# Performance work log

Hardware: AMD Instinct MI355X
Metric: run time of the kernel (lower is better)

The kernel has to match this reference:

```python
import jax, jax.numpy as jnp
import numpy as np
from jax import lax

B_SZ, C_IN, C_OUT, H_IM, W_IM = 2, 128, 128, 64, 64
N_STATE = 16
DT_RANK = 4  # ceil(128/32)


def _ln_cf(x, w, b, eps=1e-6):
    # channels_first LayerNorm over channel dim
    u = x.mean(1, keepdims=True)
    s = ((x - u) ** 2).mean(1, keepdims=True)
    return w[None, :, None, None] * (x - u) / jnp.sqrt(s + eps) + b[None, :, None, None]


def _bn_train(x, g, b, eps=1e-5):
    # BatchNorm2d in training mode (batch statistics, biased variance)
    m = x.mean((0, 2, 3), keepdims=True)
    v = ((x - m) ** 2).mean((0, 2, 3), keepdims=True)
    return g[None, :, None, None] * (x - m) / jnp.sqrt(v + eps) + b[None, :, None, None]


def _dwconv(x, w, b):
    y = lax.conv_general_dilated(x, w, (1, 1), 'SAME', feature_group_count=x.shape[1],
                                 dimension_numbers=('NCHW', 'OIHW', 'NCHW'))
    return y + b[None, :, None, None]


def _conv1x1(x, w, b):
    return jnp.einsum('oi,bihw->bohw', w, x) + b[None, :, None, None]


def _selective_scan(u, dt, A, Bm, Cm, D, delta_bias):
    # u, dt: [B,Ch,L]; A: [Ch,N]; Bm, Cm: [B,N,L]; D: [Ch]
    dt = jax.nn.softplus(dt + delta_bias[None, :, None])
    xs = (dt.transpose(2, 0, 1), u.transpose(2, 0, 1), Bm.transpose(2, 0, 1), Cm.transpose(2, 0, 1))
    h0 = jnp.zeros(u.shape[:2] + (A.shape[1],), u.dtype)

    def step(h, inp):
        dt_t, u_t, b_t, c_t = inp
        dA = jnp.exp(dt_t[..., None] * A)                        # [B,Ch,N]
        h = h * dA + (dt_t * u_t)[..., None] * b_t[:, None, :]   # [B,Ch,N]
        return h, jnp.einsum('bcn,bn->bc', h, c_t)

    _, ys = lax.scan(step, h0, xs)
    return ys.transpose(1, 2, 0) + u * D[None, :, None]


def _ssm_apply(u, Wx, bx, Wdt, bdt, Alog, D, r):
    # u: [B,Ch,L]. Replicates torch row-major .reshape of [(B L),D] -> [B,D,L].
    Bb, Ch, L = u.shape
    N = Alog.shape[1]
    x_flat = u.transpose(0, 2, 1).reshape(Bb * L, Ch)   # 'b c l -> (b l) c'
    x_dbl = x_flat @ Wx.T + bx
    dt = (x_dbl[:, :r] @ Wdt.T + bdt).reshape(Bb, Wdt.shape[0], L)
    Bm = x_dbl[:, r:r + N].reshape(Bb, N, L)
    Cm = x_dbl[:, r + N:].reshape(Bb, N, L)
    return _selective_scan(u, dt, -jnp.exp(Alog), Bm, Cm, D, bdt)


def _forward(x, ln_in_w, ln_in_b, inproj_w, inproj_b, ln_mamba_w, ln_mamba_b, convm_w, convm_b,
             convr_w, convr_b, ln_cat_w, ln_cat_b, xproj_f_w, xproj_f_b, dtproj_f_w, dtproj_f_b,
             Alog_f, D_f, xproj_b_w, xproj_b_b, dtproj_b_w, dtproj_b_b, Alog_b, D_b,
             xproj_u_w, xproj_u_b, dtproj_u_w, dtproj_u_b, Alog_u, D_u, gate1_w, gate1_b,
             bn_g, bn_b, gate2_w, gate2_b, outproj_w, outproj_b, outln_w, outln_b):
    Bb, C, H, W = x.shape
    L = H * W
    half = C // 2
    x = _ln_cf(x, ln_in_w, ln_in_b)
    xp = _conv1x1(x, inproj_w, inproj_b)
    x_mamba, x_res = xp[:, :C], xp[:, C:]
    x_mamba = _ln_cf(x_mamba, ln_mamba_w, ln_mamba_b)
    x_mamba = jax.nn.silu(_dwconv(x_mamba, convm_w, convm_b))
    x_res = jax.nn.silu(_dwconv(x_res, convr_w, convr_b))
    # forward scan on first half of channels
    xf = x_mamba[:, :half].reshape(Bb, half, L)
    yf = _ssm_apply(xf, xproj_f_w, xproj_f_b, dtproj_f_w, dtproj_f_b, Alog_f, D_f, DT_RANK).reshape(Bb, half, H, W)
    # backward scan on second half (flip H,W, scan, flip back)
    xb = x_mamba[:, half:][:, :, ::-1, ::-1]
    yb = _ssm_apply(xb.reshape(Bb, half, L), xproj_b_w, xproj_b_b, dtproj_b_w, dtproj_b_b,
                    Alog_b, D_b, DT_RANK).reshape(Bb, half, H, W)[:, :, ::-1, ::-1]
    concat = _ln_cf(jnp.concatenate([yf, yb], axis=1), ln_cat_w, ln_cat_b)
    # uncertainty-ordered scan on full x_mamba
    sig = jax.nn.sigmoid(x_mamba.mean(1, keepdims=True))
    unc = (-(sig * jnp.log(sig + 1e-6))).reshape(Bb, L)
    idx = jnp.argsort(-unc, axis=1)       # descending uncertainty
    inv = jnp.argsort(idx, axis=1)        # inverse permutation
    xs = jnp.take_along_axis(x_mamba.reshape(Bb, C, L), idx[:, None, :], axis=2)
    yu = _ssm_apply(xs, xproj_u_w, xproj_u_b, dtproj_u_w, dtproj_u_b, Alog_u, D_u, 2 * DT_RANK)
    yu = jnp.take_along_axis(yu, inv[:, None, :], axis=2).reshape(Bb, C, H, W)
    # gated fusion
    g = jax.nn.relu(_bn_train(_conv1x1(jnp.concatenate([concat, yu], 1), gate1_w, gate1_b), bn_g, bn_b))
    g = jax.nn.sigmoid(_conv1x1(g, gate2_w, gate2_b))
    fused = g * yu + (1.0 - g) * concat
    out = _conv1x1(jnp.concatenate([fused, x_res], 1), outproj_w, outproj_b)
    return _ln_cf(out, outln_w, outln_b)


def setup_inputs() -> dict:
    key = jax.random.key(0)
    ks = jax.random.split(key, 16)
    C, half, R, N = C_IN, C_IN // 2, DT_RANK, N_STATE
    rn = lambda k, shp, s=0.02: jax.random.normal(k, shp, jnp.float32) * s

    def inv_dt(k, n):
        dt = jnp.exp(jax.random.uniform(k, (n,)) * (np.log(0.1) - np.log(0.001)) + np.log(0.001))
        dt = jnp.maximum(dt, 1e-4)
        return dt + jnp.log(-jnp.expm1(-dt))

    std = R ** -0.5
    Alog_h = jnp.log(jnp.broadcast_to(jnp.arange(1, N + 1, dtype=jnp.float32), (half, N)))
    Alog_fl = jnp.log(jnp.broadcast_to(jnp.arange(1, N + 1, dtype=jnp.float32), (C, N)))
    return {
        'x': jax.random.normal(ks[0], (B_SZ, C, H_IM, W_IM), jnp.float32),
        'ln_in_w': jnp.ones(C), 'ln_in_b': jnp.zeros(C),
        'inproj_w': rn(ks[1], (2 * C, C)), 'inproj_b': jnp.zeros(2 * C),
        'ln_mamba_w': jnp.ones(C), 'ln_mamba_b': jnp.zeros(C),
        'convm_w': rn(ks[2], (C, 1, 3, 3), 0.1), 'convm_b': jnp.zeros(C),
        'convr_w': rn(ks[3], (C, 1, 3, 3), 0.1), 'convr_b': jnp.zeros(C),
        'ln_cat_w': jnp.ones(C), 'ln_cat_b': jnp.zeros(C),
        'xproj_f_w': rn(ks[4], (R + 2 * N, half)), 'xproj_f_b': jnp.zeros(R + 2 * N),
        'dtproj_f_w': jax.random.uniform(ks[5], (half, R), minval=-std, maxval=std),
        'dtproj_f_b': inv_dt(ks[6], half),
        'Alog_f': Alog_h, 'D_f': jnp.ones(half),
        'xproj_b_w': rn(ks[7], (R + 2 * N, half)), 'xproj_b_b': jnp.zeros(R + 2 * N),
        'dtproj_b_w': jax.random.uniform(ks[8], (half, R), minval=-std, maxval=std),
        'dtproj_b_b': inv_dt(ks[9], half),
        'Alog_b': Alog_h, 'D_b': jnp.ones(half),
        'xproj_u_w': rn(ks[10], (2 * R + 2 * N, C)), 'xproj_u_b': jnp.zeros(2 * R + 2 * N),
        'dtproj_u_w': jax.random.uniform(ks[11], (C, 2 * R), minval=-std, maxval=std),
        'dtproj_u_b': inv_dt(ks[12], C),
        'Alog_u': Alog_fl, 'D_u': jnp.ones(C),
        'gate1_w': rn(ks[13], (C, 2 * C)), 'gate1_b': jnp.zeros(C),
        'bn_g': jnp.ones(C), 'bn_b': jnp.zeros(C),
        'gate2_w': rn(ks[14], (C, C)), 'gate2_b': jnp.zeros(C),
        'outproj_w': rn(ks[15], (C_OUT, 2 * C)), 'outproj_b': jnp.zeros(C_OUT),
        'outln_w': jnp.ones(C_OUT), 'outln_b': jnp.zeros(C_OUT),
    }


def reference(x, ln_in_w, ln_in_b, inproj_w, inproj_b, ln_mamba_w, ln_mamba_b, convm_w, convm_b,
              convr_w, convr_b, ln_cat_w, ln_cat_b, xproj_f_w, xproj_f_b, dtproj_f_w, dtproj_f_b,
              Alog_f, D_f, xproj_b_w, xproj_b_b, dtproj_b_w, dtproj_b_b, Alog_b, D_b,
              xproj_u_w, xproj_u_b, dtproj_u_w, dtproj_u_b, Alog_u, D_u, gate1_w, gate1_b,
              bn_g, bn_b, gate2_w, gate2_b, outproj_w, outproj_b, outln_w, outln_b):
    return _forward(x, ln_in_w, ln_in_b, inproj_w, inproj_b, ln_mamba_w, ln_mamba_b, convm_w, convm_b,
                    convr_w, convr_b, ln_cat_w, ln_cat_b, xproj_f_w, xproj_f_b, dtproj_f_w, dtproj_f_b,
                    Alog_f, D_f, xproj_b_w, xproj_b_b, dtproj_b_w, dtproj_b_b, Alog_b, D_b,
                    xproj_u_w, xproj_u_b, dtproj_u_w, dtproj_u_b, Alog_u, D_u, gate1_w, gate1_b,
                    bn_g, bn_b, gate2_w, gate2_b, outproj_w, outproj_b, outln_w, outln_b)
```

## Files before the change

### kernel.cpp

```cpp
#include <hip/hip_runtime.h>
#include <cstdint>
#include <cstddef>

#define TPB 256

namespace {

constexpr int B_SZ = 2;
constexpr int C    = 128;
constexpr int HALF = 64;
constexpr int L    = 4096;
constexpr int N    = 16;
constexpr int HH   = 64;
constexpr int WW   = 64;

__device__ __forceinline__ float softplusf(float x) {
  return fmaxf(x, 0.f) + __logf(1.f + __expf(-fabsf(x)));
}
__device__ __forceinline__ float sigm(float x) { return 1.f / (1.f + __expf(-x)); }

__device__ __forceinline__ unsigned long long unc_key(float u, int i) {
  unsigned m = __float_as_uint(u);
  m = (m & 0x80000000u) ? ~m : (m | 0x80000000u);
  return ((unsigned long long)(~m) << 32) | (unsigned)i;
}

__global__ void k_conv_ln(const float* __restrict__ X, int bsX,
                          const float* __restrict__ lnw, const float* __restrict__ lnb,
                          const float* __restrict__ W, const float* __restrict__ bias,
                          float* __restrict__ Y, int I, int O,
                          float* __restrict__ st1s, float* __restrict__ st1q) {
  constexpr int O_PB = 8;
  __shared__ float Wl[O_PB * 128];
  __shared__ float aw[128], ab[128];
  const int o0 = blockIdx.y * O_PB;
  const int b  = blockIdx.z;
  for (int t = threadIdx.x; t < O_PB * I; t += TPB) {
    int i = t / O_PB, k = t % O_PB;
    Wl[t] = W[(size_t)(o0 + k) * I + i];
  }
  for (int t = threadIdx.x; t < I; t += TPB) { aw[t] = lnw[t]; ab[t] = lnb[t]; }
  __syncthreads();
  const int l0 = blockIdx.x * (2 * TPB) + threadIdx.x;
  const int l1 = l0 + TPB;
  const float* X0 = X + (size_t)b * bsX + l0;
  const float* X1 = X + (size_t)b * bsX + l1;
  float s0 = 0.f, q0 = 0.f, s1 = 0.f, q1 = 0.f;
#pragma unroll 8
  for (int i = 0; i < I; ++i) {
    float v0 = X0[(size_t)i * L], v1 = X1[(size_t)i * L];
    s0 += v0; q0 += v0 * v0; s1 += v1; q1 += v1 * v1;
  }
  const float m0 = s0 / I, m1 = s1 / I;
  const float r0 = rsqrtf(q0 / I - m0 * m0 + 1e-6f);
  const float r1 = rsqrtf(q1 / I - m1 * m1 + 1e-6f);
  float acc0[O_PB], acc1[O_PB];
#pragma unroll
  for (int k = 0; k < O_PB; ++k) { acc0[k] = bias[o0 + k]; acc1[k] = acc0[k]; }
#pragma unroll 4
  for (int i = 0; i < I; ++i) {
    float xv0 = (X0[(size_t)i * L] - m0) * r0 * aw[i] + ab[i];
    float xv1 = (X1[(size_t)i * L] - m1) * r1 * aw[i] + ab[i];
#pragma unroll
    for (int k = 0; k < O_PB; ++k) {
      acc0[k] += Wl[i * O_PB + k] * xv0;
      acc1[k] += Wl[i * O_PB + k] * xv1;
    }
  }
#pragma unroll
  for (int k = 0; k < O_PB; ++k) {
    Y[((size_t)b * O + o0 + k) * L + l0] = acc0[k];
    Y[((size_t)b * O + o0 + k) * L + l1] = acc1[k];
  }
  if (o0 < 128) {
    float ss0 = 0.f, qq0 = 0.f, ss1 = 0.f, qq1 = 0.f;
#pragma unroll
    for (int k = 0; k < O_PB; ++k) {
      ss0 += acc0[k]; qq0 += acc0[k] * acc0[k];
      ss1 += acc1[k]; qq1 += acc1[k] * acc1[k];
    }
    atomicAdd(&st1s[b * L + l0], ss0);
    atomicAdd(&st1q[b * L + l0], qq0);
    atomicAdd(&st1s[b * L + l1], ss1);
    atomicAdd(&st1q[b * L + l1], qq1);
  }
}

__global__ void k_dwconv_t(const float* __restrict__ xp,
                           const float* __restrict__ st1s, const float* __restrict__ st1q,
                           const float* __restrict__ lnw, const float* __restrict__ lnb,
                           const float* __restrict__ Wm, const float* __restrict__ bm,
                           const float* __restrict__ Wr, const float* __restrict__ br,
                           float* __restrict__ xm, float* __restrict__ xr) {
  const int c = blockIdx.y;
  const int z = blockIdx.z;
  const int b = z & 1, mode = z >> 1;
  const int h0 = blockIdx.x * 4;
  __shared__ float T[6][66];
  const float* Xc = xp + ((size_t)b * 2 * C + (mode ? C + c : c)) * L;
  const float lw = mode ? 0.f : lnw[c];
  const float lb2 = mode ? 0.f : lnb[c];
  for (int t = threadIdx.x; t < 6 * 66; t += TPB) {
    int r = t / 66, cc = t % 66 - 1;
    int hh = h0 - 1 + r;
    float v = 0.f;
    if (hh >= 0 && hh < HH && cc >= 0 && cc < WW) {
      int li = hh * WW + cc;
      v = Xc[li];
      if (mode == 0) {
        float sv = st1s[b * L + li], qv = st1q[b * L + li];
        float m = sv * (1.f / 128.f);
        float rr = rsqrtf(qv * (1.f / 128.f) - m * m + 1e-6f);
        v = (v - m) * rr * lw + lb2;
      }
    }
    T[r][t % 66] = v;
  }
  __syncthreads();
  const int hl = threadIdx.x >> 6, w = threadIdx.x & 63;
  const float* W9 = (mode ? Wr : Wm) + c * 9;
  float acc = mode ? br[c] : bm[c];
#pragma unroll
  for (int kh = 0; kh < 3; ++kh)
#pragma unroll
    for (int kw = 0; kw < 3; ++kw)
      acc += T[hl + kh][w + kw] * W9[kh * 3 + kw];
  const int l = (h0 + hl) * WW + w;
  float* Yp = mode ? xr : xm;
  Yp[((size_t)b * C + c) * L + l] = acc * sigm(acc);
}

__global__ void k_unc(const float* __restrict__ xm, float* __restrict__ unc) {
  const int lp = threadIdx.x & 31;
  const int g  = threadIdx.x >> 5;
  const int p  = blockIdx.x * 32 + lp;
  const int b = p / L, l = p % L;
  const float* Xp = xm + (size_t)b * C * L + l;
  float s = 0.f;
#pragma unroll 8
  for (int i = 0; i < 16; ++i) s += Xp[(size_t)(g * 16 + i) * L];
  __shared__ float r1[8][32];
  r1[g][lp] = s;
  __syncthreads();
  if (g == 0) {
    float st = 0.f;
#pragma unroll
    for (int j = 0; j < 8; ++j) st += r1[j][lp];
    float sg = sigm(st / C);
    unc[p] = -(sg * __logf(sg + 1e-6f));
  }
}

__global__ void k_rank(const float* __restrict__ unc, int* __restrict__ rankbuf) {
  constexpr int JC = 512;
  __shared__ unsigned long long K[JC];
  const int b  = blockIdx.z;
  const int j0 = blockIdx.y * JC;
  const int i  = blockIdx.x * TPB + threadIdx.x;
  for (int t = threadIdx.x; t < JC; t += TPB)
    K[t] = unc_key(unc[b * L + j0 + t], j0 + t);
  __syncthreads();
  const unsigned long long my = unc_key(unc[b * L + i], i);
  int cnt = 0;
#pragma unroll 8
  for (int j = 0; j < JC; ++j) cnt += (K[j] < my) ? 1 : 0;
  atomicAdd(&rankbuf[b * L + i], cnt);
}

__global__ void k_scatgath(const float* __restrict__ xm, const int* __restrict__ rankbuf,
                           float* __restrict__ xs, int* __restrict__ inv,
                           int* __restrict__ idx) {
  int t = blockIdx.x * TPB + threadIdx.x;
  int l = t % L, c = (t / L) % C, b = t / (C * L);
  int r = rankbuf[b * L + l];
  xs[((size_t)b * C + c) * L + r] = xm[t];
  if (c == 0) { inv[b * L + l] = r; idx[b * L + r] = l; }
}

__global__ void k_convx_all(const float* __restrict__ xm, const float* __restrict__ xs,
                            const float* __restrict__ Wf, const float* __restrict__ bf,
                            const float* __restrict__ Wb, const float* __restrict__ bb,
                            const float* __restrict__ Wu, const float* __restrict__ bu,
                            float* __restrict__ XDF, float* __restrict__ XDU) {
  constexpr int O_PB = 8;
  const int z = blockIdx.z;
  const bool isU = z >= 4;
  const int I = isU ? 128 : 64;
  const int O = isU ? 40 : 36;
  const int o0 = blockIdx.y * O_PB;
  if (o0 >= O) return;
  int b, dir;
  const float *W, *bi;
  if (!isU) { dir = z >> 1; b = z & 1; W = dir ? Wb : Wf; bi = dir ? bb : bf; }
  else      { dir = 0; b = z - 4; W = Wu; bi = bu; }
  __shared__ float Wl[O_PB * 128];
  for (int t = threadIdx.x; t < O_PB * I; t += TPB) {
    int i = t / O_PB, k = t % O_PB;
    Wl[t] = (o0 + k < O) ? W[(size_t)(o0 + k) * I + i] : 0.f;
  }
  __syncthreads();
  const int l = blockIdx.x * TPB + threadIdx.x;
  const int ls = isU ? l : (dir ? (L - 1 - l) : l);
  const float* Xb = isU ? (xs + (size_t)b * C * L)
                        : (xm + ((size_t)b * C + dir * HALF) * L);
  float acc[O_PB];
#pragma unroll
  for (int k = 0; k < O_PB; ++k) acc[k] = (o0 + k < O) ? bi[o0 + k] : 0.f;
#pragma unroll 4
  for (int i = 0; i < I; ++i) {
    float xv = Xb[(size_t)i * L + ls];
#pragma unroll
    for (int k = 0; k < O_PB; ++k) acc[k] += Wl[i * O_PB + k] * xv;
  }
  float* yp = isU ? (XDU + ((size_t)b * L + l) * 40 + o0)
                  : (XDF + ((size_t)z * L + l) * 36 + o0);
#pragma unroll
  for (int k = 0; k < O_PB; ++k)
    if (o0 + k < O) yp[k] = acc[k];
}

__global__ void k_bc_all(const float* __restrict__ xdblF, const float* __restrict__ xdblU,
                         float* __restrict__ BmTF, float* __restrict__ CmTF,
                         float* __restrict__ BmTU, float* __restrict__ CmTU) {
  const int z = blockIdx.z;
  const bool isU = z >= 4;
  const int RT = isU ? 8 : 4, OT = isU ? 40 : 36;
  const float* src = isU ? (xdblU + (size_t)(z - 4) * L * 40)
                         : (xdblF + (size_t)z * L * 36);
  float* BT = isU ? (BmTU + (size_t)(z - 4) * L * N) : (BmTF + (size_t)z * L * N);
  float* CT = isU ? (CmTU + (size_t)(z - 4) * L * N) : (CmTF + (size_t)z * L * N);
  const int n = blockIdx.y;
  const int l2 = blockIdx.x * TPB + threadIdx.x;
  int f2 = n * L + l2;
  int lb = f2 >> 4, cb = f2 & 15;
  const float* xr2 = src + (size_t)lb * OT + RT + cb;
  size_t ob = (size_t)l2 * N + n;
  BT[ob] = xr2[0];
  CT[ob] = xr2[N];
}

__global__ __launch_bounds__(1024) void
k_scan_all(const float* __restrict__ xdblF, const float* __restrict__ xdblU,
           const float* __restrict__ dtf_w, const float* __restrict__ dtf_b,
           const float* __restrict__ dtb_w, const float* __restrict__ dtb_b,
           const float* __restrict__ dtu_w, const float* __restrict__ dtu_b,
           const float* __restrict__ xm, const float* __restrict__ xs,
           const int* __restrict__ idx,
           const float* __restrict__ BmTF, const float* __restrict__ CmTF,
           const float* __restrict__ BmTU, const float* __restrict__ CmTU,
           const float* __restrict__ Alog_f, const float* __restrict__ Alog_b,
           const float* __restrict__ Alog_u,
           const float* __restrict__ D_f, const float* __restrict__ D_b,
           const float* __restrict__ D_u,
           float* __restrict__ yf, float* __restrict__ yb, float* __restrict__ yu) {
  const int blk = blockIdx.x;
  const int tid = threadIdx.x;
  const bool isU = blk >= 256;
  int CsT, RT, c, b, dir;
  const float *Wdt, *bdt, *Alog, *Dv, *xdbl, *BT, *CT, *Ub;
  const int* idxb = nullptr;
  float* Y;
  int OT;
  if (!isU) {
    CsT = 64; RT = 4; OT = 36;
    int zb = blk >> 6; c = blk & 63; dir = zb >> 1; b = zb & 1;
    Wdt = dir ? dtb_w : dtf_w; bdt = dir ? dtb_b : dtf_b;
    Alog = dir ? Alog_b : Alog_f; Dv = dir ? D_b : D_f;
    xdbl = xdblF + (size_t)zb * L * 36;
    BT = BmTF + (size_t)zb * L * N; CT = CmTF + (size_t)zb * L * N;
    Ub = xm + ((size_t)b * C + dir * HALF + c) * L;
    Y = (dir ? yb : yf) + ((size_t)b * HALF + c) * L;
  } else {
    CsT = 128; RT = 8; OT = 40;
    int blk2 = blk - 256; b = blk2 >> 7; c = blk2 & 127; dir = 0;
    Wdt = dtu_w; bdt = dtu_b; Alog = Alog_u; Dv = D_u;
    xdbl = xdblU + (size_t)b * L * 40;
    BT = BmTU + (size_t)b * L * N; CT = CmTU + (size_t)b * L * N;
    Ub = xs + ((size_t)b * C + c) * L;
    idxb = idx + b * L;
    Y = yu + ((size_t)b * C + c) * L;
  }
  __shared__ float sW[1024];
  __shared__ float sb2[128];
  __shared__ float4 dtL4[64 * 17];
  __shared__ float4 uL4[64 * 17];
  __shared__ float sA[N][65], sH[N][65];
  for (int t = tid; t < CsT * RT; t += 1024) {
    int csrc = t / RT, r = t % RT;
    sW[r * CsT + csrc] = Wdt[t];
  }
  for (int t = tid; t < CsT; t += 1024) sb2[t] = bdt[t];
  __syncthreads();
  {
    const int chunk_d = tid >> 4;
    const int sq4 = tid & 15;
    const int sq = sq4 * 4;
    const int lsrc = isU ? (c * 32 + (chunk_d >> 1)) : (c * 64 + chunk_d);
    const float* xrp = xdbl + (size_t)lsrc * OT;
    float xr[8];
    for (int r = 0; r < RT; ++r) xr[r] = xrp[r];
    const float bcc = sb2[c];
    float dv[4], uv[4];
#pragma unroll
    for (int j = 0; j < 4; ++j) {
      int s = sq + j;
      int csrc = isU ? (((chunk_d & 1) << 6) + s) : s;
      float acc = sb2[csrc] + bcc;
      for (int r = 0; r < RT; ++r) acc += sW[r * CsT + csrc] * xr[r];
      int l = (chunk_d << 6) + s;
      dv[j] = softplusf(acc);
      uv[j] = Ub[isU ? l : (dir ? (L - 1 - l) : l)];
    }
    dtL4[chunk_d * 17 + sq4] = make_float4(dv[0], dv[1], dv[2], dv[3]);
    uL4[chunk_d * 17 + sq4]  = make_float4(uv[0], uv[1], uv[2], uv[3]);
  }
  __syncthreads();
  const int n = tid & 15;
  const int chunk = tid >> 4;
  const float a = -__expf(Alog[c * N + n]);
  const float* bp = BT + ((size_t)(chunk << 6)) * N + n;
  const float* cp = CT + ((size_t)(chunk << 6)) * N + n;
  float ap = 1.f, h = 0.f;
#pragma unroll 4
  for (int m = 0; m < 16; ++m) {
    float4 d4 = dtL4[chunk * 17 + m];
    float4 u4 = uL4[chunk * 17 + m];
    float dv[4] = {d4.x, d4.y, d4.z, d4.w};
    float uv[4] = {u4.x, u4.y, u4.z, u4.w};
#pragma unroll
    for (int jj = 0; jj < 4; ++jj) {
      int s = (m << 2) + jj;
      float bn = bp[(size_t)s * N];
      float dA = __expf(dv[jj] * a);
      ap *= dA;
      h = h * dA + dv[jj] * uv[jj] * bn;
    }
  }
  sA[n][chunk] = ap; sH[n][chunk] = h;
  __syncthreads();
  {
    const int w = tid >> 6;
    const int k = tid & 63;
    float A = sA[w][k];
    float Bv = sH[w][k];
#pragma unroll
    for (int j = 1; j < 64; j <<= 1) {
      float pa = __shfl_up(A, j);
      float pb = __shfl_up(Bv, j);
      if (k >= j) { Bv = pb * A + Bv; A = pa * A; }
    }
    float hprev = __shfl_up(Bv, 1);
    sH[w][k] = (k == 0) ? 0.f : hprev;
  }
  __syncthreads();
  h = sH[n][chunk];
  const float Dc = Dv[c];
  const float* uLrow = (const float*)&uL4[chunk * 17];
  const bool h1 = (n & 1) != 0, h2 = (n & 2) != 0, h3 = (n & 4) != 0, h4 = (n & 8) != 0;
  float ybuf[4];
#pragma unroll
  for (int q = 0; q < 4; ++q) {
    float v[16];
#pragma unroll
    for (int m = 0; m < 4; ++m) {
      float4 d4 = dtL4[chunk * 17 + (q << 2) + m];
      float4 u4 = uL4[chunk * 17 + (q << 2) + m];
      float dv[4] = {d4.x, d4.y, d4.z, d4.w};
      float uv[4] = {u4.x, u4.y, u4.z, u4.w};
#pragma unroll
      for (int jj = 0; jj < 4; ++jj) {
        int s = (q << 4) + (m << 2) + jj;
        float bn = bp[(size_t)s * N];
        float cn = cp[(size_t)s * N];
        float dA = __expf(dv[jj] * a);
        h = h * dA + dv[jj] * uv[jj] * bn;
        v[(m << 2) + jj] = h * cn;
      }
    }
    float u8[8];
#pragma unroll
    for (int k2 = 0; k2 < 8; ++k2) {
      float snd = h1 ? v[2 * k2] : v[2 * k2 + 1];
      float t = __shfl_xor(snd, 1);
      u8[k2] = (h1 ? v[2 * k2 + 1] : v[2 * k2]) + t;
    }
    float u4a[4];
#pragma unroll
    for (int k2 = 0; k2 < 4; ++k2) {
      float snd = h2 ? u8[2 * k2] : u8[2 * k2 + 1];
      float t = __shfl_xor(snd, 2);
      u4a[k2] = (h2 ? u8[2 * k2 + 1] : u8[2 * k2]) + t;
    }
    float u2a[2];
#pragma unroll
    for (int k2 = 0; k2 < 2; ++k2) {
      float snd = h3 ? u4a[2 * k2] : u4a[2 * k2 + 1];
      float t = __shfl_xor(snd, 4);
      u2a[k2] = (h3 ? u4a[2 * k2 + 1] : u4a[2 * k2]) + t;
    }
    float snd = h4 ? u2a[0] : u2a[1];
    float t = __shfl_xor(snd, 8);
    float ysum = (h4 ? u2a[1] : u2a[0]) + t;
    float myu = uLrow[(q << 4) + n];
    ybuf[q] = ysum + myu * Dc;
  }
  if (!isU) {
    float* Yp = Y + (chunk << 6);
#pragma unroll
    for (int q = 0; q < 4; ++q) Yp[16 * q + n] = ybuf[q];
  } else {
    const int s0 = chunk << 6;
#pragma unroll
    for (int q = 0; q < 4; ++q) Y[idxb[s0 + 16 * q + n]] = ybuf[q];
  }
}

template <int O_PB>
__global__ void k_gate1(const float* __restrict__ yf, const float* __restrict__ yb,
                        const float* __restrict__ lncw, const float* __restrict__ lncb,
                        const float* __restrict__ yu,
                        const float* __restrict__ W, const float* __restrict__ bias,
                        float* __restrict__ g1,
                        float* __restrict__ st2m, float* __restrict__ st2r,
                        float* __restrict__ bnsum) {
  __shared__ float Wl[O_PB * 256];
  __shared__ float cw[128], cb2[128];
  __shared__ float part[2][O_PB][4];
  const int o0 = blockIdx.y * O_PB;
  const int b  = blockIdx.z;
  for (int t = threadIdx.x; t < O_PB * 256; t += TPB) {
    int i = t / O_PB, k = t % O_PB;
    Wl[t] = W[(size_t)(o0 + k) * 256 + i];
  }
  for (int t = threadIdx.x; t < 128; t += TPB) { cw[t] = lncw[t]; cb2[t] = lncb[t]; }
  __syncthreads();
  const int l = blockIdx.x * TPB + threadIdx.x;
  const float* f0 = yf + (size_t)b * HALF * L + l;
  const float* b0 = yb + (size_t)b * HALF * L + (L - 1 - l);
  const float* u0 = yu + (size_t)b * C * L + l;
  float s = 0.f, s2 = 0.f;
#pragma unroll 8
  for (int i = 0; i < 64; ++i) { float v = f0[(size_t)i * L]; s += v; s2 += v * v; }
#pragma unroll 8
  for (int i = 0; i < 64; ++i) { float v = b0[(size_t)i * L]; s += v; s2 += v * v; }
  const float m = s / C;
  const float r = rsqrtf(s2 / C - m * m + 1e-6f);
  if (blockIdx.y == 0) { st2m[b * L + l] = m; st2r[b * L + l] = r; }
  float acc[O_PB];
#pragma unroll
  for (int k = 0; k < O_PB; ++k) acc[k] = bias[o0 + k];
#pragma unroll 4
  for (int i = 0; i < 64; ++i) {
    float cv = (f0[(size_t)i * L] - m) * r * cw[i] + cb2[i];
#pragma unroll
    for (int k = 0; k < O_PB; ++k) acc[k] += Wl[i * O_PB + k] * cv;
  }
#pragma unroll 4
  for (int i = 0; i < 64; ++i) {
    float cv = (b0[(size_t)i * L] - m) * r * cw[64 + i] + cb2[64 + i];
#pragma unroll
    for (int k = 0; k < O_PB; ++k) acc[k] += Wl[(64 + i) * O_PB + k] * cv;
  }
#pragma unroll 4
  for (int i = 0; i < 128; ++i) {
    float xv = u0[(size_t)i * L];
#pragma unroll
    for (int k = 0; k < O_PB; ++k) acc[k] += Wl[(128 + i) * O_PB + k] * xv;
  }
#pragma unroll
  for (int k = 0; k < O_PB; ++k)
    g1[((size_t)b * C + o0 + k) * L + l] = acc[k];
  const int wv = threadIdx.x >> 6, lnn = threadIdx.x & 63;
#pragma unroll
  for (int k = 0; k < O_PB; ++k) {
    float v = acc[k];
    v += __shfl_xor(v, 1);  v += __shfl_xor(v, 2);  v += __shfl_xor(v, 4);
    v += __shfl_xor(v, 8);  v += __shfl_xor(v, 16); v += __shfl_xor(v, 32);
    if (lnn == 0) part[0][k][wv] = v;
    float q = acc[k] * acc[k];
    q += __shfl_xor(q, 1);  q += __shfl_xor(q, 2);  q += __shfl_xor(q, 4);
    q += __shfl_xor(q, 8);  q += __shfl_xor(q, 16); q += __shfl_xor(q, 32);
    if (lnn == 0) part[1][k][wv] = q;
  }
  __syncthreads();
  if (threadIdx.x < 2 * O_PB) {
    int which = threadIdx.x >= O_PB, k = threadIdx.x % O_PB;
    float v = part[which][k][0] + part[which][k][1] + part[which][k][2] + part[which][k][3];
    atomicAdd(&bnsum[which * 128 + o0 + k], v);
  }
}

template <int O_PB>
__global__ void k_gate2_fuse(const float* __restrict__ g1,
                             const float* __restrict__ bnsum,
                             const float* __restrict__ bn_g, const float* __restrict__ bn_b,
                             const float* __restrict__ W, const float* __restrict__ bias,
                             const float* __restrict__ yu,
                             const float* __restrict__ yf, const float* __restrict__ yb,
                             const float* __restrict__ mean2, const float* __restrict__ rinv2,
                             const float* __restrict__ lncw, const float* __restrict__ lncb,
                             float* __restrict__ fused) {
  __shared__ float Wl[O_PB * 128];
  __shared__ float sc[128], sh[128];
  __shared__ float cwo[O_PB], cbo[O_PB];
  const int o0 = blockIdx.y * O_PB;
  const int b  = blockIdx.z;
  for (int t = threadIdx.x; t < O_PB * 128; t += TPB) {
    int i = t / O_PB, k = t % O_PB;
    Wl[t] = W[(size_t)(o0 + k) * 128 + i];
  }
  for (int t = threadIdx.x; t < 128; t += TPB) {
    float sv = bnsum[t], qv = bnsum[128 + t];
    float mean = sv / (B_SZ * L);
    float var  = qv / (B_SZ * L) - mean * mean;
    float scv = bn_g[t] * rsqrtf(var + 1e-5f);
    sc[t] = scv;
    sh[t] = bn_b[t] - mean * scv;
  }
  if (threadIdx.x < O_PB) {
    cwo[threadIdx.x] = lncw[o0 + threadIdx.x];
    cbo[threadIdx.x] = lncb[o0 + threadIdx.x];
  }
  __syncthreads();
  const int l = blockIdx.x * TPB + threadIdx.x;
  const float m = mean2[b * L + l], r = rinv2[b * L + l];
  const float* Xb = g1 + (size_t)b * C * L + l;
  float acc[O_PB];
#pragma unroll
  for (int k = 0; k < O_PB; ++k) acc[k] = bias[o0 + k];
#pragma unroll 4
  for (int i = 0; i < 128; ++i) {
    float v = fmaxf(Xb[(size_t)i * L] * sc[i] + sh[i], 0.f);
#pragma unroll
    for (int k = 0; k < O_PB; ++k) acc[k] += Wl[i * O_PB + k] * v;
  }
#pragma unroll
  for (int k = 0; k < O_PB; ++k) {
    int o = o0 + k;
    float g = sigm(acc[k]);
    float yuv = yu[((size_t)b * C + o) * L + l];
    float yv = (o < 64) ? yf[((size_t)b * HALF + o) * L + l]
                        : yb[((size_t)b * HALF + (o - 64)) * L + (L - 1 - l)];
    float cv = (yv - m) * r * cwo[k] + cbo[k];
    fused[((size_t)b * C + o) * L + l] = g * yuv + (1.f - g) * cv;
  }
}

template <int O_PB>
__global__ void k_conv1x1_cat2(const float* __restrict__ X1, const float* __restrict__ X2,
                               const float* __restrict__ W, const float* __restrict__ bias,
                               float* __restrict__ Y, int O,
                               float* __restrict__ st3s, float* __restrict__ st3q) {
  __shared__ float Wl[O_PB * 256];
  const int o0 = blockIdx.y * O_PB;
  const int b  = blockIdx.z;
  for (int t = threadIdx.x; t < O_PB * 256; t += TPB) {
    int i = t / O_PB, k = t % O_PB;
    Wl[t] = W[(size_t)(o0 + k) * 256 + i];
  }
  __syncthreads();
  const int l = blockIdx.x * TPB + threadIdx.x;
  const float* Xb1 = X1 + (size_t)b * C * L + l;
  const float* Xb2 = X2 + (size_t)b * C * L + l;
  float acc[O_PB];
#pragma unroll
  for (int k = 0; k < O_PB; ++k) acc[k] = bias[o0 + k];
#pragma unroll 4
  for (int i = 0; i < 128; ++i) {
    float xv = Xb1[(size_t)i * L];
#pragma unroll
    for (int k = 0; k < O_PB; ++k) acc[k] += Wl[i * O_PB + k] * xv;
  }
#pragma unroll 4
  for (int i = 0; i < 128; ++i) {
    float xv = Xb2[(size_t)i * L];
#pragma unroll
    for (int k = 0; k < O_PB; ++k) acc[k] += Wl[(128 + i) * O_PB + k] * xv;
  }
#pragma unroll
  for (int k = 0; k < O_PB; ++k)
    Y[((size_t)b * O + o0 + k) * L + l] = acc[k];
  float ss = 0.f, qq = 0.f;
#pragma unroll
  for (int k = 0; k < O_PB; ++k) { ss += acc[k]; qq += acc[k] * acc[k]; }
  atomicAdd(&st3s[b * L + l], ss);
  atomicAdd(&st3q[b * L + l], qq);
}

__global__ void k_ln_fin(const float* __restrict__ X,
                         const float* __restrict__ st3s, const float* __restrict__ st3q,
                         const float* __restrict__ w, const float* __restrict__ bchan,
                         float* __restrict__ Y) {
  int t = blockIdx.x * TPB + threadIdx.x;
  int l = t % L, c = (t / L) % C, b = t / (C * L);
  float m = st3s[b * L + l] * (1.f / 128.f);
  float rinv = rsqrtf(st3q[b * L + l] * (1.f / 128.f) - m * m + 1e-6f);
  Y[t] = w[c] * (X[t] - m) * rinv + bchan[c];
}

}

extern "C" void kernel_launch(void* const* d_in, const int* in_sizes, int n_in,
                              void* d_out, int out_size, void* d_ws, size_t ws_size,
                              hipStream_t stream) {
  const float* x         = (const float*)d_in[0];
  const float* ln_in_w   = (const float*)d_in[1];
  const float* ln_in_b   = (const float*)d_in[2];
  const float* inproj_w  = (const float*)d_in[3];
  const float* inproj_b  = (const float*)d_in[4];
  const float* ln_m_w    = (const float*)d_in[5];
  const float* ln_m_b    = (const float*)d_in[6];
  const float* convm_w   = (const float*)d_in[7];
  const float* convm_b   = (const float*)d_in[8];
  const float* convr_w   = (const float*)d_in[9];
  const float* convr_b   = (const float*)d_in[10];
  const float* ln_cat_w  = (const float*)d_in[11];
  const float* ln_cat_b  = (const float*)d_in[12];
  const float* xpf_w     = (const float*)d_in[13];
  const float* xpf_b     = (const float*)d_in[14];
  const float* dtf_w     = (const float*)d_in[15];
  const float* dtf_b     = (const float*)d_in[16];
  const float* Alog_f    = (const float*)d_in[17];
  const float* D_f       = (const float*)d_in[18];
  const float* xpb_w     = (const float*)d_in[19];
  const float* xpb_b     = (const float*)d_in[20];
  const float* dtb_w     = (const float*)d_in[21];
  const float* dtb_b     = (const float*)d_in[22];
  const float* Alog_b    = (const float*)d_in[23];
  const float* D_b       = (const float*)d_in[24];
  const float* xpu_w     = (const float*)d_in[25];
  const float* xpu_b     = (const float*)d_in[26];
  const float* dtu_w     = (const float*)d_in[27];
  const float* dtu_b     = (const float*)d_in[28];
  const float* Alog_u    = (const float*)d_in[29];
  const float* D_u       = (const float*)d_in[30];
  const float* gate1_w   = (const float*)d_in[31];
  const float* gate1_b   = (const float*)d_in[32];
  const float* bn_g      = (const float*)d_in[33];
  const float* bn_b      = (const float*)d_in[34];
  const float* gate2_w   = (const float*)d_in[35];
  const float* gate2_b   = (const float*)d_in[36];
  const float* outproj_w = (const float*)d_in[37];
  const float* outproj_b = (const float*)d_in[38];
  const float* outln_w   = (const float*)d_in[39];
  const float* outln_b   = (const float*)d_in[40];

  float* ws = (float*)d_ws;
  size_t off = 0;
  auto alloc = [&](size_t n) { float* p = ws + off; off += n; return p; };

  const size_t BL = (size_t)B_SZ * L;
  float* st1s  = alloc(BL);
  float* st1q  = alloc(BL);
  int*   rank  = (int*)alloc(BL);
  float* st3s  = alloc(BL);
  float* st3q  = alloc(BL);
  float* bnsum = alloc(256);
  const size_t zeroBytes = (5 * BL + 256) * sizeof(float);

  float* xp    = alloc((size_t)B_SZ * 2 * C * L);
  float* xm    = alloc((size_t)B_SZ * C * L);
  float* xr    = alloc((size_t)B_SZ * C * L);
  float* unc   = alloc(BL);
  int*   inv   = (int*)alloc(BL);
  int*   idx   = (int*)alloc(BL);
  float* xs    = alloc((size_t)B_SZ * C * L);
  float* xdblF = alloc((size_t)4 * L * 36);
  float* BmTF  = alloc((size_t)4 * L * N);
  float* CmTF  = alloc((size_t)4 * L * N);
  float* xdblU = alloc((size_t)2 * L * 40);
  float* BmTU  = alloc((size_t)2 * L * N);
  float* CmTU  = alloc((size_t)2 * L * N);
  float* yf    = alloc((size_t)B_SZ * HALF * L);
  float* yb    = alloc((size_t)B_SZ * HALF * L);
  float* yu    = alloc((size_t)B_SZ * C * L);
  float* st2m  = alloc(BL);
  float* st2r  = alloc(BL);
  float* g1    = alloc((size_t)B_SZ * C * L);
  float* fused = alloc((size_t)B_SZ * C * L);
  float* outp  = alloc((size_t)B_SZ * C * L);
  (void)ws_size; (void)in_sizes; (void)n_in; (void)out_size;

  const int elemB = B_SZ * C * L / TPB;

  hipMemsetAsync(st1s, 0, zeroBytes, stream);
  k_conv_ln<<<dim3(L / (2 * TPB), 32, B_SZ), TPB, 0, stream>>>(
      x, C * L, ln_in_w, ln_in_b, inproj_w, inproj_b, xp, 128, 256, st1s, st1q);
  k_dwconv_t<<<dim3(HH / 4, C, 2 * B_SZ), TPB, 0, stream>>>(
      xp, st1s, st1q, ln_m_w, ln_m_b, convm_w, convm_b, convr_w, convr_b, xm, xr);
  k_unc<<<B_SZ * L / 32, TPB, 0, stream>>>(xm, unc);
  k_rank<<<dim3(L / TPB, 8, B_SZ), TPB, 0, stream>>>(unc, rank);
  k_scatgath<<<elemB, TPB, 0, stream>>>(xm, rank, xs, inv, idx);
  k_convx_all<<<dim3(L / TPB, 5, 6), TPB, 0, stream>>>(
      xm, xs, xpf_w, xpf_b, xpb_w, xpb_b, xpu_w, xpu_b, xdblF, xdblU);
  k_bc_all<<<dim3(L / TPB, N, 6), TPB, 0, stream>>>(
      xdblF, xdblU, BmTF, CmTF, BmTU, CmTU);
  k_scan_all<<<512, 1024, 0, stream>>>(
      xdblF, xdblU, dtf_w, dtf_b, dtb_w, dtb_b, dtu_w, dtu_b,
      xm, xs, idx, BmTF, CmTF, BmTU, CmTU,
      Alog_f, Alog_b, Alog_u, D_f, D_b, D_u, yf, yb, yu);
  k_gate1<8><<<dim3(L / TPB, 16, B_SZ), TPB, 0, stream>>>(
      yf, yb, ln_cat_w, ln_cat_b, yu, gate1_w, gate1_b, g1, st2m, st2r, bnsum);
  k_gate2_fuse<8><<<dim3(L / TPB, 16, B_SZ), TPB, 0, stream>>>(
      g1, bnsum, bn_g, bn_b, gate2_w, gate2_b, yu, yf, yb, st2m, st2r,
      ln_cat_w, ln_cat_b, fused);
  k_conv1x1_cat2<8><<<dim3(L / TPB, 16, B_SZ), TPB, 0, stream>>>(
      fused, xr, outproj_w, outproj_b, outp, 128, st3s, st3q);
  k_ln_fin<<<elemB, TPB, 0, stream>>>(outp, st3s, st3q, outln_w, outln_b,
                                      (float*)d_out);
}
```

Before: 330.1 us.

## Merge sort pipeline and epilogue stages into cooperative kernels with grid sync

Measured after the change: 743.3 us. +125.2%, slower.

```diff
diff --git a/kernel.cpp b/kernel.cpp
--- a/kernel.cpp
+++ b/kernel.cpp
@@ -1,8 +1,11 @@
 #include <hip/hip_runtime.h>
+#include <hip/hip_cooperative_groups.h>
 #include <cstdint>
 #include <cstddef>
 
 #define TPB 256
+
+namespace cg = cooperative_groups;
 
 namespace {
 
@@ -130,51 +133,58 @@
   Yp[((size_t)b * C + c) * L + l] = acc * sigm(acc);
 }
 
-__global__ void k_unc(const float* __restrict__ xm, float* __restrict__ unc) {
-  const int lp = threadIdx.x & 31;
-  const int g  = threadIdx.x >> 5;
-  const int p  = blockIdx.x * 32 + lp;
-  const int b = p / L, l = p % L;
-  const float* Xp = xm + (size_t)b * C * L + l;
-  float s = 0.f;
+__global__ void k_sortpipe(const float* __restrict__ xm, float* __restrict__ unc,
+                           int* __restrict__ rankbuf, float* __restrict__ xs,
+                           int* __restrict__ inv, int* __restrict__ idx) {
+  cg::grid_group grid = cg::this_grid();
+  const int tid = threadIdx.x;
+  const int blk = blockIdx.x;
+  {
+    const int lp = tid & 31;
+    const int g  = tid >> 5;
+    const int p  = blk * 32 + lp;
+    const int b = p / L, l = p % L;
+    const float* Xp = xm + (size_t)b * C * L + l;
+    float s = 0.f;
 #pragma unroll 8
-  for (int i = 0; i < 16; ++i) s += Xp[(size_t)(g * 16 + i) * L];
-  __shared__ float r1[8][32];
-  r1[g][lp] = s;
-  __syncthreads();
-  if (g == 0) {
-    float st = 0.f;
-#pragma unroll
-    for (int j = 0; j < 8; ++j) st += r1[j][lp];
-    float sg = sigm(st / C);
-    unc[p] = -(sg * __logf(sg + 1e-6f));
-  }
-}
-
-__global__ void k_rank(const float* __restrict__ unc, int* __restrict__ rankbuf) {
-  constexpr int JC = 512;
-  __shared__ unsigned long long K[JC];
-  const int b  = blockIdx.z;
-  const int j0 = blockIdx.y * JC;
-  const int i  = blockIdx.x * TPB + threadIdx.x;
-  for (int t = threadIdx.x; t < JC; t += TPB)
-    K[t] = unc_key(unc[b * L + j0 + t], j0 + t);
-  __syncthreads();
-  const unsigned long long my = unc_key(unc[b * L + i], i);
-  int cnt = 0;
+    for (int i = 0; i < 16; ++i) s += Xp[(size_t)(g * 16 + i) * L];
+    __shared__ float r1[8][32];
+    r1[g][lp] = s;
+    __syncthreads();
+    if (g == 0) {
+      float st = 0.f;
+#pragma unroll
+      for (int j = 0; j < 8; ++j) st += r1[j][lp];
+      float sg = sigm(st / C);
+      unc[p] = -(sg * __logf(sg + 1e-6f));
+    }
+  }
+  __threadfence();
+  grid.sync();
+  {
+    const int b  = blk >> 7;
+    const int xg = blk & 15;
+    const int jy = (blk >> 4) & 7;
+    const int j0 = jy * 512;
+    const int i  = xg * TPB + tid;
+    __shared__ unsigned long long K[512];
+    for (int t = tid; t < 512; t += TPB)
+      K[t] = unc_key(unc[b * L + j0 + t], j0 + t);
+    __syncthreads();
+    const unsigned long long my = unc_key(unc[b * L + i], i);
+    int cnt = 0;
 #pragma unroll 8
-  for (int j = 0; j < JC; ++j) cnt += (K[j] < my) ? 1 : 0;
-  atomicAdd(&rankbuf[b * L + i], cnt);
-}
-
-__global__ void k_scatgath(const float* __restrict__ xm, const int* __restrict__ rankbuf,
-                           float* __restrict__ xs, int* __restrict__ inv,
-                           int* __restrict__ idx) {
-  int t = blockIdx.x * TPB + threadIdx.x;
-  int l = t % L, c = (t / L) % C, b = t / (C * L);
-  int r = rankbuf[b * L + l];
-  xs[((size_t)b * C + c) * L + r] = xm[t];
-  if (c == 0) { inv[b * L + l] = r; idx[b * L + r] = l; }
+    for (int j = 0; j < 512; ++j) cnt += (K[j] < my) ? 1 : 0;
+    atomicAdd(&rankbuf[b * L + i], cnt);
+  }
+  __threadfence();
+  grid.sync();
+  for (int t = blk * TPB + tid; t < B_SZ * C * L; t += 256 * TPB) {
+    int l = t % L, c = (t / L) % C, b = t / (C * L);
+    int r = rankbuf[b * L + l];
+    xs[((size_t)b * C + c) * L + r] = xm[t];
+    if (c == 0) { inv[b * L + l] = r; idx[b * L + r] = l; }
+  }
 }
 
 __global__ void k_convx_all(const float* __restrict__ xm, const float* __restrict__ xs,
@@ -415,187 +425,185 @@
   }
 }
 
-template <int O_PB>
-__global__ void k_gate1(const float* __restrict__ yf, const float* __restrict__ yb,
-                        const float* __restrict__ lncw, const float* __restrict__ lncb,
-                        const float* __restrict__ yu,
-                        const float* __restrict__ W, const float* __restrict__ bias,
-                        float* __restrict__ g1,
-                        float* __restrict__ st2m, float* __restrict__ st2r,
-                        float* __restrict__ bnsum) {
-  __shared__ float Wl[O_PB * 256];
-  __shared__ float cw[128], cb2[128];
-  __shared__ float part[2][O_PB][4];
-  const int o0 = blockIdx.y * O_PB;
-  const int b  = blockIdx.z;
-  for (int t = threadIdx.x; t < O_PB * 256; t += TPB) {
-    int i = t / O_PB, k = t % O_PB;
-    Wl[t] = W[(size_t)(o0 + k) * 256 + i];
-  }
-  for (int t = threadIdx.x; t < 128; t += TPB) { cw[t] = lncw[t]; cb2[t] = lncb[t]; }
-  __syncthreads();
-  const int l = blockIdx.x * TPB + threadIdx.x;
-  const float* f0 = yf + (size_t)b * HALF * L + l;
-  const float* b0 = yb + (size_t)b * HALF * L + (L - 1 - l);
-  const float* u0 = yu + (size_t)b * C * L + l;
-  float s = 0.f, s2 = 0.f;
+__global__ void k_epilogue(const float* __restrict__ yf, const float* __restrict__ yb,
+                           const float* __restrict__ lncw, const float* __restrict__ lncb,
+                           const float* __restrict__ yu,
+                           const float* __restrict__ g1w, const float* __restrict__ g1b,
+                           float* __restrict__ g1,
+                           float* __restrict__ st2m, float* __restrict__ st2r,
+                           float* __restrict__ bnsum,
+                           const float* __restrict__ bn_g, const float* __restrict__ bn_b,
+                           const float* __restrict__ g2w, const float* __restrict__ g2b,
+                           float* __restrict__ fused,
+                           const float* __restrict__ xr,
+                           const float* __restrict__ opw, const float* __restrict__ opb,
+                           float* __restrict__ outp,
+                           float* __restrict__ st3s, float* __restrict__ st3q,
+                           const float* __restrict__ olnw, const float* __restrict__ olnb,
+                           float* __restrict__ OUT) {
+  cg::grid_group grid = cg::this_grid();
+  constexpr int O_PB = 8;
+  const int xb = blockIdx.x & 15;
+  const int yb2 = (blockIdx.x >> 4) & 15;
+  const int b  = blockIdx.x >> 8;
+  const int o0 = yb2 * O_PB;
+  const int l  = xb * TPB + threadIdx.x;
+
+  {
+    __shared__ float Wl[O_PB * 256];
+    __shared__ float cw[128], cb2[128];
+    __shared__ float part[2][O_PB][4];
+    for (int t = threadIdx.x; t < O_PB * 256; t += TPB) {
+      int i = t / O_PB, k = t % O_PB;
+      Wl[t] = g1w[(size_t)(o0 + k) * 256 + i];
+    }
+    for (int t = threadIdx.x; t < 128; t += TPB) { cw[t] = lncw[t]; cb2[t] = lncb[t]; }
+    __syncthreads();
+    const float* f0 = yf + (size_t)b * HALF * L + l;
+    const float* b0 = yb + (size_t)b * HALF * L + (L - 1 - l);
+    const float* u0 = yu + (size_t)b * C * L + l;
+    float s = 0.f, s2 = 0.f;
 #pragma unroll 8
-  for (int i = 0; i < 64; ++i) { float v = f0[(size_t)i * L]; s += v; s2 += v * v; }
+    for (int i = 0; i < 64; ++i) { float v = f0[(size_t)i * L]; s += v; s2 += v * v; }
 #pragma unroll 8
-  for (int i = 0; i < 64; ++i) { float v = b0[(size_t)i * L]; s += v; s2 += v * v; }
-  const float m = s / C;
-  const float r = rsqrtf(s2 / C - m * m + 1e-6f);
-  if (blockIdx.y == 0) { st2m[b * L + l] = m; st2r[b * L + l] = r; }
-  float acc[O_PB];
-#pragma unroll
-  for (int k = 0; k < O_PB; ++k) acc[k] = bias[o0 + k];
-#pragma unroll 4
-  for (int i = 0; i < 64; ++i) {
-    float cv = (f0[(size_t)i * L] - m) * r * cw[i] + cb2[i];
-#pragma unroll
-    for (int k = 0; k < O_PB; ++k) acc[k] += Wl[i * O_PB + k] * cv;
-  }
-#pragma unroll 4
-  for (int i = 0; i < 64; ++i) {
-    float cv = (b0[(size_t)i * L] - m) * r * cw[64 + i] + cb2[64 + i];
-#pragma unroll
-    for (int k = 0; k < O_PB; ++k) acc[k] += Wl[(64 + i) * O_PB + k] * cv;
-  }
-#pragma unroll 4
-  for (int i = 0; i < 128; ++i) {
-    float xv = u0[(size_t)i * L];
-#pragma unroll
-    for (int k = 0; k < O_PB; ++k) acc[k] += Wl[(128 + i) * O_PB + k] * xv;
-  }
-#pragma unroll
-  for (int k = 0; k < O_PB; ++k)
-    g1[((size_t)b * C + o0 + k) * L + l] = acc[k];
-  const int wv = threadIdx.x >> 6, lnn = threadIdx.x & 63;
-#pragma unroll
-  for (int k = 0; k < O_PB; ++k) {
-    float v = acc[k];
-    v += __shfl_xor(v, 1);  v += __shfl_xor(v, 2);  v += __shfl_xor(v, 4);
-    v += __shfl_xor(v, 8);  v += __shfl_xor(v, 16); v += __shfl_xor(v, 32);
-    if (lnn == 0) part[0][k][wv] = v;
-    float q = acc[k] * acc[k];
-    q += __shfl_xor(q, 1);  q += __shfl_xor(q, 2);  q += __shfl_xor(q, 4);
-    q += __shfl_xor(q, 8);  q += __shfl_xor(q, 16); q += __shfl_xor(q, 32);
-    if (lnn == 0) part[1][k][wv] = q;
-  }
-  __syncthreads();
-  if (threadIdx.x < 2 * O_PB) {
-    int which = threadIdx.x >= O_PB, k = threadIdx.x % O_PB;
-    float v = part[which][k][0] + part[which][k][1] + part[which][k][2] + part[which][k][3];
-    atomicAdd(&bnsum[which * 128 + o0 + k], v);
-  }
-}
-
-template <int O_PB>
-__global__ void k_gate2_fuse(const float* __restrict__ g1,
-                             const float* __restrict__ bnsum,
-                             const float* __restrict__ bn_g, const float* __restrict__ bn_b,
-                             const float* __restrict__ W, const float* __restrict__ bias,
-                             const float* __restrict__ yu,
-                             const float* __restrict__ yf, const float* __restrict__ yb,
-                             const float* __restrict__ mean2, const float* __restrict__ rinv2,
-                             const float* __restrict__ lncw, const float* __restrict__ lncb,
-                             float* __restrict__ fused) {
-  __shared__ float Wl[O_PB * 128];
-  __shared__ float sc[128], sh[128];
-  __shared__ float cwo[O_PB], cbo[O_PB];
-  const int o0 = blockIdx.y * O_PB;
-  const int b  = blockIdx.z;
-  for (int t = threadIdx.x; t < O_PB * 128; t += TPB) {
-    int i = t / O_PB, k = t % O_PB;
-    Wl[t] = W[(size_t)(o0 + k) * 128 + i];
-  }
-  for (int t = threadIdx.x; t < 128; t += TPB) {
-    float sv = bnsum[t], qv = bnsum[128 + t];
-    float mean = sv / (B_SZ * L);
-    float var  = qv / (B_SZ * L) - mean * mean;
-    float scv = bn_g[t] * rsqrtf(var + 1e-5f);
-    sc[t] = scv;
-    sh[t] = bn_b[t] - mean * scv;
-  }
-  if (threadIdx.x < O_PB) {
-    cwo[threadIdx.x] = lncw[o0 + threadIdx.x];
-    cbo[threadIdx.x] = lncb[o0 + threadIdx.x];
-  }
-  __syncthreads();
-  const int l = blockIdx.x * TPB + threadIdx.x;
-  const float m = mean2[b * L + l], r = rinv2[b * L + l];
-  const float* Xb = g1 + (size_t)b * C * L + l;
-  float acc[O_PB];
-#pragma unroll
-  for (int k = 0; k < O_PB; ++k) acc[k] = bias[o0 + k];
-#pragma unroll 4
-  for (int i = 0; i < 128; ++i) {
-    float v = fmaxf(Xb[(size_t)i * L] * sc[i] + sh[i], 0.f);
-#pragma unroll
-    for (int k = 0; k < O_PB; ++k) acc[k] += Wl[i * O_PB + k] * v;
-  }
-#pragma unroll
-  for (int k = 0; k < O_PB; ++k) {
-    int o = o0 + k;
-    float g = sigm(acc[k]);
-    float yuv = yu[((size_t)b * C + o) * L + l];
-    float yv = (o < 64) ? yf[((size_t)b * HALF + o) * L + l]
-                        : yb[((size_t)b * HALF + (o - 64)) * L + (L - 1 - l)];
-    float cv = (yv - m) * r * cwo[k] + cbo[k];
-    fused[((size_t)b * C + o) * L + l] = g * yuv + (1.f - g) * cv;
-  }
-}
-
-template <int O_PB>
-__global__ void k_conv1x1_cat2(const float* __restrict__ X1, const float* __restrict__ X2,
-                               const float* __restrict__ W, const float* __restrict__ bias,
-                               float* __restrict__ Y, int O,
-                               float* __restrict__ st3s, float* __restrict__ st3q) {
-  __shared__ float Wl[O_PB * 256];
-  const int o0 = blockIdx.y * O_PB;
-  const int b  = blockIdx.z;
-  for (int t = threadIdx.x; t < O_PB * 256; t += TPB) {
-    int i = t / O_PB, k = t % O_PB;
-    Wl[t] = W[(size_t)(o0 + k) * 256 + i];
-  }
-  __syncthreads();
-  const int l = blockIdx.x * TPB + threadIdx.x;
-  const float* Xb1 = X1 + (size_t)b * C * L + l;
-  const float* Xb2 = X2 + (size_t)b * C * L + l;
-  float acc[O_PB];
-#pragma unroll
-  for (int k = 0; k < O_PB; ++k) acc[k] = bias[o0 + k];
-#pragma unroll 4
-  for (int i = 0; i < 128; ++i) {
-    float xv = Xb1[(size_t)i * L];
-#pragma unroll
-    for (int k = 0; k < O_PB; ++k) acc[k] += Wl[i * O_PB + k] * xv;
-  }
-#pragma unroll 4
-  for (int i = 0; i < 128; ++i) {
-    float xv = Xb2[(size_t)i * L];
-#pragma unroll
-    for (int k = 0; k < O_PB; ++k) acc[k] += Wl[(128 + i) * O_PB + k] * xv;
-  }
-#pragma unroll
-  for (int k = 0; k < O_PB; ++k)
-    Y[((size_t)b * O + o0 + k) * L + l] = acc[k];
-  float ss = 0.f, qq = 0.f;
-#pragma unroll
-  for (int k = 0; k < O_PB; ++k) { ss += acc[k]; qq += acc[k] * acc[k]; }
-  atomicAdd(&st3s[b * L + l], ss);
-  atomicAdd(&st3q[b * L + l], qq);
-}
-
-__global__ void k_ln_fin(const float* __restrict__ X,
-                         const float* __restrict__ st3s, const float* __restrict__ st3q,
-                         const float* __restrict__ w, const float* __restrict__ bchan,
-                         float* __restrict__ Y) {
-  int t = blockIdx.x * TPB + threadIdx.x;
-  int l = t % L, c = (t / L) % C, b = t / (C * L);
-  float m = st3s[b * L + l] * (1.f / 128.f);
-  float rinv = rsqrtf(st3q[b * L + l] * (1.f / 128.f) - m * m + 1e-6f);
-  Y[t] = w[c] * (X[t] - m) * rinv + bchan[c];
+    for (int i = 0; i < 64; ++i) { float v = b0[(size_t)i * L]; s += v; s2 += v * v; }
+    const float m = s / C;
+    const float r = rsqrtf(s2 / C - m * m + 1e-6f);
+    if (yb2 == 0) { st2m[b * L + l] = m; st2r[b * L + l] = r; }
+    float acc[O_PB];
+#pragma unroll
+    for (int k = 0; k < O_PB; ++k) acc[k] = g1b[o0 + k];
+#pragma unroll 4
+    for (int i = 0; i < 64; ++i) {
+      float cv = (f0[(size_t)i * L] - m) * r * cw[i] + cb2[i];
+#pragma unroll
+      for (int k = 0; k < O_PB; ++k) acc[k] += Wl[i * O_PB + k] * cv;
+    }
+#pragma unroll 4
+    for (int i = 0; i < 64; ++i) {
+      float cv = (b0[(size_t)i * L] - m) * r * cw[64 + i] + cb2[64 + i];
+#pragma unroll
+      for (int k = 0; k < O_PB; ++k) acc[k] += Wl[(64 + i) * O_PB + k] * cv;
+    }
+#pragma unroll 4
+    for (int i = 0; i < 128; ++i) {
+      float xv = u0[(size_t)i * L];
+#pragma unroll
+      for (int k = 0; k < O_PB; ++k) acc[k] += Wl[(128 + i) * O_PB + k] * xv;
+    }
+#pragma unroll
+    for (int k = 0; k < O_PB; ++k)
+      g1[((size_t)b * C + o0 + k) * L + l] = acc[k];
+    const int wv = threadIdx.x >> 6, lnn = threadIdx.x & 63;
+#pragma unroll
+    for (int k = 0; k < O_PB; ++k) {
+      float v = acc[k];
+      v += __shfl_xor(v, 1);  v += __shfl_xor(v, 2);  v += __shfl_xor(v, 4);
+      v += __shfl_xor(v, 8);  v += __shfl_xor(v, 16); v += __shfl_xor(v, 32);
+      if (lnn == 0) part[0][k][wv] = v;
+      float q = acc[k] * acc[k];
+      q += __shfl_xor(q, 1);  q += __shfl_xor(q, 2);  q += __shfl_xor(q, 4);
+      q += __shfl_xor(q, 8);  q += __shfl_xor(q, 16); q += __shfl_xor(q, 32);
+      if (lnn == 0) part[1][k][wv] = q;
+    }
+    __syncthreads();
+    if (threadIdx.x < 2 * O_PB) {
+      int which = threadIdx.x >= O_PB, k = threadIdx.x % O_PB;
+      float v = part[which][k][0] + part[which][k][1] + part[which][k][2] + part[which][k][3];
+      atomicAdd(&bnsum[which * 128 + o0 + k], v);
+    }
+  }
+  __threadfence();
+  grid.sync();
+
+  {
+    __shared__ float Wl2[O_PB * 128];
+    __shared__ float sc[128], sh[128];
+    __shared__ float cwo[O_PB], cbo[O_PB];
+    for (int t = threadIdx.x; t < O_PB * 128; t += TPB) {
+      int i = t / O_PB, k = t % O_PB;
+      Wl2[t] = g2w[(size_t)(o0 + k) * 128 + i];
+    }
+    for (int t = threadIdx.x; t < 128; t += TPB) {
+      float sv = bnsum[t], qv = bnsum[128 + t];
+      float mean = sv / (B_SZ * L);
+      float var  = qv / (B_SZ * L) - mean * mean;
+      float scv = bn_g[t] * rsqrtf(var + 1e-5f);
+      sc[t] = scv;
+      sh[t] = bn_b[t] - mean * scv;
+    }
+    if (threadIdx.x < O_PB) {
+      cwo[threadIdx.x] = lncw[o0 + threadIdx.x];
+      cbo[threadIdx.x] = lncb[o0 + threadIdx.x];
+    }
+    __syncthreads();
+    const float m = st2m[b * L + l], r = st2r[b * L + l];
+    const float* Xb = g1 + (size_t)b * C * L + l;
+    float acc[O_PB];
+#pragma unroll
+    for (int k = 0; k < O_PB; ++k) acc[k] = g2b[o0 + k];
+#pragma unroll 4
+    for (int i = 0; i < 128; ++i) {
+      float v = fmaxf(Xb[(size_t)i * L] * sc[i] + sh[i], 0.f);
+#pragma unroll
+      for (int k = 0; k < O_PB; ++k) acc[k] += Wl2[i * O_PB + k] * v;
+    }
+#pragma unroll
+    for (int k = 0; k < O_PB; ++k) {
+      int o = o0 + k;
+      float g = sigm(acc[k]);
+      float yuv = yu[((size_t)b * C + o) * L + l];
+      float yv = (o < 64) ? yf[((size_t)b * HALF + o) * L + l]
+                          : yb[((size_t)b * HALF + (o - 64)) * L + (L - 1 - l)];
+      float cv = (yv - m) * r * cwo[k] + cbo[k];
+      fused[((size_t)b * C + o) * L + l] = g * yuv + (1.f - g) * cv;
+    }
+  }
+  __threadfence();
+  grid.sync();
+
+  {
+    __shared__ float Wl3[O_PB * 256];
+    for (int t = threadIdx.x; t < O_PB * 256; t += TPB) {
+      int i = t / O_PB, k = t % O_PB;
+      Wl3[t] = opw[(size_t)(o0 + k) * 256 + i];
+    }
+    __syncthreads();
+    const float* Xb1 = fused + (size_t)b * C * L + l;
+    const float* Xb2 = xr + (size_t)b * C * L + l;
+    float acc[O_PB];
+#pragma unroll
+    for (int k = 0; k < O_PB; ++k) acc[k] = opb[o0 + k];
+#pragma unroll 4
+    for (int i = 0; i < 128; ++i) {
+      float xv = Xb1[(size_t)i * L];
+#pragma unroll
+      for (int k = 0; k < O_PB; ++k) acc[k] += Wl3[i * O_PB + k] * xv;
+    }
+#pragma unroll 4
+    for (int i = 0; i < 128; ++i) {
+      float xv = Xb2[(size_t)i * L];
+#pragma unroll
+      for (int k = 0; k < O_PB; ++k) acc[k] += Wl3[(128 + i) * O_PB + k] * xv;
+    }
+#pragma unroll
+    for (int k = 0; k < O_PB; ++k)
+      outp[((size_t)b * C + o0 + k) * L + l] = acc[k];
+    float ss = 0.f, qq = 0.f;
+#pragma unroll
+    for (int k = 0; k < O_PB; ++k) { ss += acc[k]; qq += acc[k] * acc[k]; }
+    atomicAdd(&st3s[b * L + l], ss);
+    atomicAdd(&st3q[b * L + l], qq);
+  }
+  __threadfence();
+  grid.sync();
+
+  for (int t = blockIdx.x * TPB + threadIdx.x; t < B_SZ * C * L; t += 512 * TPB) {
+    int ll = t % L, cc = (t / L) % C, bb = t / (C * L);
+    float m = st3s[bb * L + ll] * (1.f / 128.f);
+    float rinv = rsqrtf(st3q[bb * L + ll] * (1.f / 128.f) - m * m + 1e-6f);
+    OUT[t] = olnw[cc] * (outp[t] - m) * rinv + olnb[cc];
+  }
 }
 
 }
@@ -679,18 +687,20 @@
   float* g1    = alloc((size_t)B_SZ * C * L);
   float* fused = alloc((size_t)B_SZ * C * L);
   float* outp  = alloc((size_t)B_SZ * C * L);
+  float* outF  = (float*)d_out;
   (void)ws_size; (void)in_sizes; (void)n_in; (void)out_size;
-
-  const int elemB = B_SZ * C * L / TPB;
 
   hipMemsetAsync(st1s, 0, zeroBytes, stream);
   k_conv_ln<<<dim3(L / (2 * TPB), 32, B_SZ), TPB, 0, stream>>>(
       x, C * L, ln_in_w, ln_in_b, inproj_w, inproj_b, xp, 128, 256, st1s, st1q);
   k_dwconv_t<<<dim3(HH / 4, C, 2 * B_SZ), TPB, 0, stream>>>(
       xp, st1s, st1q, ln_m_w, ln_m_b, convm_w, convm_b, convr_w, convr_b, xm, xr);
-  k_unc<<<B_SZ * L / 32, TPB, 0, stream>>>(xm, unc);
-  k_rank<<<dim3(L / TPB, 8, B_SZ), TPB, 0, stream>>>(unc, rank);
-  k_scatgath<<<elemB, TPB, 0, stream>>>(xm, rank, xs, inv, idx);
+  {
+    void* args[] = {(void*)&xm, (void*)&unc, (void*)&rank, (void*)&xs,
+                    (void*)&inv, (void*)&idx};
+    hipLaunchCooperativeKernel((const void*)k_sortpipe, dim3(256), dim3(TPB),
+                               args, 0, stream);
+  }
   k_convx_all<<<dim3(L / TPB, 5, 6), TPB, 0, stream>>>(
       xm, xs, xpf_w, xpf_b, xpb_w, xpb_b, xpu_w, xpu_b, xdblF, xdblU);
   k_bc_all<<<dim3(L / TPB, N, 6), TPB, 0, stream>>>(
@@ -699,13 +709,15 @@
       xdblF, xdblU, dtf_w, dtf_b, dtb_w, dtb_b, dtu_w, dtu_b,
       xm, xs, idx, BmTF, CmTF, BmTU, CmTU,
       Alog_f, Alog_b, Alog_u, D_f, D_b, D_u, yf, yb, yu);
-  k_gate1<8><<<dim3(L / TPB, 16, B_SZ), TPB, 0, stream>>>(
-      yf, yb, ln_cat_w, ln_cat_b, yu, gate1_w, gate1_b, g1, st2m, st2r, bnsum);
-  k_gate2_fuse<8><<<dim3(L / TPB, 16, B_SZ), TPB, 0, stream>>>(
-      g1, bnsum, bn_g, bn_b, gate2_w, gate2_b, yu, yf, yb, st2m, st2r,
-      ln_cat_w, ln_cat_b, fused);
-  k_conv1x1_cat2<8><<<dim3(L / TPB, 16, B_SZ), TPB, 0, stream>>>(
-      fused, xr, outproj_w, outproj_b, outp, 128, st3s, st3q);
-  k_ln_fin<<<elemB, TPB, 0, stream>>>(outp, st3s, st3q, outln_w, outln_b,
-                                      (float*)d_out);
-}
+  {
+    void* args[] = {(void*)&yf, (void*)&yb, (void*)&ln_cat_w, (void*)&ln_cat_b,
+                    (void*)&yu, (void*)&gate1_w, (void*)&gate1_b, (void*)&g1,
+                    (void*)&st2m, (void*)&st2r, (void*)&bnsum,
+                    (void*)&bn_g, (void*)&bn_b, (void*)&gate2_w, (void*)&gate2_b,
+                    (void*)&fused, (void*)&xr, (void*)&outproj_w, (void*)&outproj_b,
+                    (void*)&outp, (void*)&st3s, (void*)&st3q,
+                    (void*)&outln_w, (void*)&outln_b, (void*)&outF};
+    hipLaunchCooperativeKernel((const void*)k_epilogue, dim3(512), dim3(TPB),
+                               args, 0, stream);
+  }
+}
```
